# Kernel optimization log

Measured on AMD Instinct MI355X. Metric: run time of the kernel, lower is better.

Reference implementation:

```python
import jax, jax.numpy as jnp
import numpy as np

N_NODES = 100000
N_EDGES = 3200000
IN_DIM, HID_DIM, OUT_DIM = 128, 64, 3


def gcn_conv(x, edge_index, W, b):
    """PyG GCNConv: add self-loops, symmetric deg^{-1/2} normalization,
    linear transform then scatter-sum aggregation, plus bias."""
    n = x.shape[0]
    loop = jnp.arange(n, dtype=edge_index.dtype)
    src = jnp.concatenate([edge_index[0], loop])  # [E+N]
    dst = jnp.concatenate([edge_index[1], loop])
    deg = jax.ops.segment_sum(jnp.ones_like(dst, dtype=x.dtype), dst, num_segments=n)
    dinv = jax.lax.rsqrt(jnp.maximum(deg, 1.0))  # deg >= 1 due to self-loops
    norm = dinv[src] * dinv[dst]                 # [E+N]
    h = x @ W                                    # [N, F_out]
    msgs = h[src] * norm[:, None]                # gather + scale
    out = jax.ops.segment_sum(msgs, dst, num_segments=n)
    return out + b


def setup_inputs() -> dict:
    key = jax.random.key(0)
    k1, k2, k3, k4 = jax.random.split(key, 4)
    x = jax.random.normal(k1, (N_NODES, IN_DIM), dtype=jnp.float32)
    edge_index = jax.random.randint(k2, (2, N_EDGES), 0, N_NODES, dtype=jnp.int64)
    W1 = jax.random.normal(k3, (IN_DIM, HID_DIM), dtype=jnp.float32) * (1.0 / np.sqrt(IN_DIM))
    b1 = jnp.zeros((HID_DIM,), dtype=jnp.float32)
    W2 = jax.random.normal(k4, (HID_DIM, OUT_DIM), dtype=jnp.float32) * (1.0 / np.sqrt(HID_DIM))
    b2 = jnp.zeros((OUT_DIM,), dtype=jnp.float32)
    return {"x": x, "edge_index": edge_index, "W1": W1, "b1": b1, "W2": W2, "b2": b2}


def reference(x, edge_index, W1, b1, W2, b2):
    h = gcn_conv(x, edge_index, W1, b1)
    h = jax.nn.relu(h)
    out = gcn_conv(h, edge_index, W2, b2)
    return out
```

## Files before the change

kernel.cpp:

```cpp
#include <hip/hip_runtime.h>
#include <hip/hip_fp16.h>
#include <cstdint>
#include <cstddef>

#define DIM_IN 128
#define DIM_HID 64
#define MS_TILE 16384
#define OVF_CAP 32768
#define BSH 9
#define BINSZ 512
#define MAXNB 512
#define CAPL 20480

typedef int v2i __attribute__((ext_vector_type(2)));

__global__ __launch_bounds__(1024) void k_msplit3(const int* __restrict__ eidx,
                                                  int* __restrict__ binCursor,
                                                  unsigned int* __restrict__ binned,
                                                  int* __restrict__ ovfCnt,
                                                  v2i* __restrict__ ovf,
                                                  int E, int NB, int cap) {
    __shared__ int hist[256], base[256];
    __shared__ int stF;
    int t = threadIdx.x;
    if (t == 0) {
        int o = 0;
        for (int j = 1; j < 128; j += 2) o |= eidx[j];
        stF = (o == 0) ? 2 : 1;
    }
    __syncthreads();
    int st = stF;
    int ntiles = (E + MS_TILE - 1) / MS_TILE;

    for (int tile = blockIdx.x; tile < ntiles; tile += gridDim.x) {
        int e0 = tile * MS_TILE;
        int e1 = min(e0 + MS_TILE, E);

        if (t < 256) hist[t] = 0;
        __syncthreads();
        for (int e = e0 + t; e < e1; e += 1024) {
            int d = (st == 2) ? ((const v2i*)eidx)[E + e].x : eidx[E + e];
            atomicAdd(&hist[d >> BSH], 1);
        }
        __syncthreads();
        if (t < NB && hist[t] > 0) base[t] = atomicAdd(&binCursor[t], hist[t]);
        __syncthreads();
        if (t < 256) hist[t] = 0;
        __syncthreads();
        for (int e = e0 + t; e < e1; e += 1024) {
            int s, d;
            if (st == 2) {
                s = ((const v2i*)eidx)[e].x;
                d = ((const v2i*)eidx)[E + e].x;
            } else {
                s = eidx[e];
                d = eidx[E + e];
            }
            int b = d >> BSH;
            int r = atomicAdd(&hist[b], 1);
            int local = base[b] + r;
            if (local < cap) {
                binned[(size_t)b * cap + local] =
                    ((unsigned int)s << BSH) | (unsigned int)(d & (BINSZ - 1));
            } else {
                int o = atomicAdd(ovfCnt, 1);
                if (o < OVF_CAP) ovf[o] = (v2i){s, d};
            }
        }
        __syncthreads();
    }
}

__global__ __launch_bounds__(512) void k_binscan(const int* __restrict__ binCursor,
                                                 int* __restrict__ binBase,
                                                 int NB, int cap) {
    __shared__ int sh[512];
    int t = threadIdx.x;
    int v = (t < NB) ? min(binCursor[t], cap) : 0;
    sh[t] = v;
    __syncthreads();
    for (int d = 1; d < 512; d <<= 1) {
        int add = (t >= d) ? sh[t - d] : 0;
        __syncthreads();
        sh[t] += add;
        __syncthreads();
    }
    if (t < NB) binBase[t] = sh[t] - v;
}

__global__ __launch_bounds__(512) void k_fillA(const unsigned int* __restrict__ binned,
                                               const int* __restrict__ binCursor,
                                               const int* __restrict__ binBase,
                                               int* __restrict__ offsets,
                                               int* __restrict__ cursor,
                                               float* __restrict__ dinv,
                                               int* __restrict__ csr,
                                               int cap, int N) {
    __shared__ int hist[BINSZ], scanS[BINSZ], curL[BINSZ];
    __shared__ unsigned int stage[CAPL];
    int b = blockIdx.x;
    int t = threadIdx.x;
    int g0 = b << BSH;
    int g = g0 + t;
    int n = min(binCursor[b], cap);
    const unsigned int* p = binned + (size_t)b * cap;

    hist[t] = 0;
    __syncthreads();
    for (int i = t; i < n; i += 512)
        atomicAdd(&hist[p[i] & (BINSZ - 1)], 1);
    __syncthreads();
    int h = hist[t];
    scanS[t] = h;
    __syncthreads();
    for (int d = 1; d < 512; d <<= 1) {
        int add = (t >= d) ? scanS[t - d] : 0;
        __syncthreads();
        scanS[t] += add;
        __syncthreads();
    }
    int excl = scanS[t] - h;
    int gbase = binBase[b];
    if (g < N) {
        offsets[g] = gbase + excl;
        dinv[g] = rsqrtf((float)(h + 1));
    }
    if (t == 511) offsets[min(g0 + BINSZ, N)] = gbase + scanS[511];

    curL[t] = excl;
    __syncthreads();
    int nl = min(n, CAPL);
    for (int i = t; i < nl; i += 512) {
        unsigned int w = p[i];
        int pos = atomicAdd(&curL[w & (BINSZ - 1)], 1);
        if (pos < CAPL) stage[pos] = w >> BSH;
    }
    __syncthreads();
    if (g < N) cursor[g] = gbase + curL[t];
    for (int i = t; i < nl; i += 512)
        csr[gbase + i] = (int)stage[i];
    __syncthreads();
    for (int i = CAPL + t; i < n; i += 512) {
        unsigned int w = p[i];
        int pos = atomicAdd(&cursor[g0 + (int)(w & (BINSZ - 1))], 1);
        csr[pos] = (int)(w >> BSH);
    }
}

__global__ void k_ovf(const int* __restrict__ ovfCnt, const v2i* __restrict__ ovf,
                      int* __restrict__ cursor, int* __restrict__ csr) {
    int n = min(*ovfCnt, OVF_CAP);
    for (int i = threadIdx.x; i < n; i += 256) {
        v2i e = ovf[i];
        int pos = atomicAdd(&cursor[e.y], 1);
        csr[pos] = e.x;
    }
}

__global__ __launch_bounds__(256) void k_gemm1t(const float* __restrict__ x,
                                                const float* __restrict__ W,
                                                const float* __restrict__ dinv,
                                                __half2* __restrict__ h1, int N) {
    __shared__ __half xsT[DIM_IN * 64];
    __shared__ float Ws[DIM_IN * DIM_HID];
    int t = threadIdx.x;
    int row0 = blockIdx.x * 64;

#pragma unroll
    for (int i = 0; i < 8; i++)
        ((float4*)Ws)[t + 256 * i] = ((const float4*)W)[t + 256 * i];

#pragma unroll
    for (int i = 0; i < 8; i++) {
        int idx = t * 8 + i;
        int r = idx >> 5;
        int kc = idx & 31;
        int row = row0 + r;
        float4 v = (row < N) ? ((const float4*)(x + (size_t)row * DIM_IN))[kc]
                             : make_float4(0.f, 0.f, 0.f, 0.f);
        xsT[(4 * kc + 0) * 64 + r] = __float2half(v.x);
        xsT[(4 * kc + 1) * 64 + r] = __float2half(v.y);
        xsT[(4 * kc + 2) * 64 + r] = __float2half(v.z);
        xsT[(4 * kc + 3) * 64 + r] = __float2half(v.w);
    }
    __syncthreads();

    int c = t & 15;
    int r = t >> 4;
    float acc[4][4] = {};

#pragma unroll 4
    for (int k = 0; k < DIM_IN; k++) {
        __half2 xh01 = *(const __half2*)&xsT[k * 64 + 4 * r];
        __half2 xh23 = *(const __half2*)&xsT[k * 64 + 4 * r + 2];
        float2 x01 = __half22float2(xh01);
        float2 x23 = __half22float2(xh23);
        float4 wb = *(const float4*)&Ws[k * DIM_HID + 4 * c];
        float xi[4] = {x01.x, x01.y, x23.x, x23.y};
#pragma unroll
        for (int i = 0; i < 4; i++) {
            acc[i][0] = fmaf(xi[i], wb.x, acc[i][0]);
            acc[i][1] = fmaf(xi[i], wb.y, acc[i][1]);
            acc[i][2] = fmaf(xi[i], wb.z, acc[i][2]);
            acc[i][3] = fmaf(xi[i], wb.w, acc[i][3]);
        }
    }

#pragma unroll
    for (int i = 0; i < 4; i++) {
        int row = row0 + 4 * r + i;
        if (row < N) {
            float d = dinv[row];
            h1[(size_t)row * 32 + 2 * c] = __floats2half2_rn(acc[i][0] * d, acc[i][1] * d);
            h1[(size_t)row * 32 + 2 * c + 1] = __floats2half2_rn(acc[i][2] * d, acc[i][3] * d);
        }
    }
}

__global__ __launch_bounds__(256) void k_agg1(const __half2* __restrict__ h1,
                                              const int* __restrict__ csr,
                                              const int* __restrict__ offsets,
                                              const float* __restrict__ dinv,
                                              const float* __restrict__ b1,
                                              const float* __restrict__ W2,
                                              float4* __restrict__ h2, int N) {
    int t = threadIdx.x;
    int hl = t & 31;
    int node = blockIdx.x * 8 + (t >> 5);
    if (node >= N) return;

    float di = dinv[node];
    int beg = offsets[node], end = offsets[node + 1];
    __half2 a0 = h1[(size_t)node * 32 + hl];
    __half2 a1 = __floats2half2_rn(0.f, 0.f);

    for (int base = beg; base < end; base += 32) {
        int rem = min(32, end - base);
        int sidx = (hl < rem) ? csr[base + hl] : 0;
        if (rem == 32) {
#pragma unroll
            for (int j0 = 0; j0 < 32; j0 += 8) {
                __half2 v[8];
#pragma unroll
                for (int k = 0; k < 8; k++) {
                    int s = __shfl(sidx, j0 + k, 32);
                    v[k] = h1[(size_t)s * 32 + hl];
                }
#pragma unroll
                for (int k = 0; k < 8; k += 2) {
                    a0 = __hadd2(a0, v[k]);
                    a1 = __hadd2(a1, v[k + 1]);
                }
            }
        } else {
            int j = 0;
            for (; j + 1 < rem; j += 2) {
                int s0 = __shfl(sidx, j, 32);
                int s1 = __shfl(sidx, j + 1, 32);
                a0 = __hadd2(a0, h1[(size_t)s0 * 32 + hl]);
                a1 = __hadd2(a1, h1[(size_t)s1 * 32 + hl]);
            }
            if (j < rem) {
                int s0 = __shfl(sidx, j, 32);
                a0 = __hadd2(a0, h1[(size_t)s0 * 32 + hl]);
            }
        }
    }

    float2 f0 = __half22float2(a0);
    float2 f1 = __half22float2(a1);
    float accx = f0.x + f1.x, accy = f0.y + f1.y;

    float2 bb = ((const float2*)b1)[hl];
    float gx = fmaxf(fmaf(accx, di, bb.x), 0.f);
    float gy = fmaxf(fmaf(accy, di, bb.y), 0.f);

    const float* w0 = W2 + (2 * hl) * 3;
    const float* w1 = W2 + (2 * hl + 1) * 3;
    float v0 = gx * w0[0] + gy * w1[0];
    float v1 = gx * w0[1] + gy * w1[1];
    float v2 = gx * w0[2] + gy * w1[2];
#pragma unroll
    for (int off = 16; off > 0; off >>= 1) {
        v0 += __shfl_xor(v0, off, 64);
        v1 += __shfl_xor(v1, off, 64);
        v2 += __shfl_xor(v2, off, 64);
    }
    if (hl == 0) h2[node] = make_float4(v0 * di, v1 * di, v2 * di, 0.f);
}

__global__ __launch_bounds__(256) void k_agg2(const float4* __restrict__ h2,
                                              const int* __restrict__ csr,
                                              const int* __restrict__ offsets,
                                              const float* __restrict__ dinv,
                                              const float* __restrict__ b2,
                                              float* __restrict__ out, int N) {
    int t = threadIdx.x;
    int l = t & 7;
    int node = blockIdx.x * 32 + (t >> 3);
    if (node >= N) return;

    float di = dinv[node];
    int beg = offsets[node], end = offsets[node + 1];
    float a0 = 0.f, a1 = 0.f, a2 = 0.f;
    for (int e = beg + l; e < end; e += 8) {
        float4 h = h2[csr[e]];
        a0 += h.x;
        a1 += h.y;
        a2 += h.z;
    }
#pragma unroll
    for (int off = 4; off > 0; off >>= 1) {
        a0 += __shfl_xor(a0, off, 8);
        a1 += __shfl_xor(a1, off, 8);
        a2 += __shfl_xor(a2, off, 8);
    }
    if (l == 0) {
        float4 hs = h2[node];
        out[(size_t)node * 3 + 0] = fmaf(a0 + hs.x, di, b2[0]);
        out[(size_t)node * 3 + 1] = fmaf(a1 + hs.y, di, b2[1]);
        out[(size_t)node * 3 + 2] = fmaf(a2 + hs.z, di, b2[2]);
    }
}

extern "C" void kernel_launch(void* const* d_in, const int* in_sizes, int n_in,
                              void* d_out, int out_size, void* d_ws, size_t ws_size,
                              hipStream_t stream) {
    const float* x = (const float*)d_in[0];
    const int* eidx = (const int*)d_in[1];
    const float* W1 = (const float*)d_in[2];
    const float* b1 = (const float*)d_in[3];
    const float* W2 = (const float*)d_in[4];
    const float* b2 = (const float*)d_in[5];
    float* out = (float*)d_out;

    const int N = in_sizes[0] / DIM_IN;
    const int E = in_sizes[1] / 2;
    const int NB = (N + BINSZ - 1) >> BSH;

    char* w = (char*)d_ws;
    size_t off = 0;
    auto carve = [&](size_t bytes) -> char* {
        char* p = w + off;
        off += (bytes + 255) & ~(size_t)255;
        return p;
    };
    int* offsets = (int*)carve((size_t)(N + 1) * 4);
    int* cursor = (int*)carve((size_t)N * 4);
    float* dinv = (float*)carve((size_t)N * 4);
    int* csr = (int*)carve((size_t)E * 4);
    int* binCursor = (int*)carve(MAXNB * 4);
    int* ovfCnt = (int*)carve(16);
    v2i* ovf = (v2i*)carve((size_t)OVF_CAP * 8);
    int* binBase = (int*)carve(MAXNB * 4);
    float4* h2 = (float4*)carve((size_t)N * 16);

    size_t h1_bytes = (size_t)N * DIM_HID * 2;
    int capDes = E / NB + E / NB / 16 + 256;
    size_t binned_des = (size_t)NB * capDes * 4;
    size_t uni_avail = (ws_size > off + 256) ? (ws_size - off - 256) : h1_bytes;
    size_t uni_bytes = binned_des > h1_bytes ? binned_des : h1_bytes;
    if (uni_bytes > uni_avail) uni_bytes = uni_avail > h1_bytes ? uni_avail : h1_bytes;
    char* uni = carve(uni_bytes);
    unsigned int* binned = (unsigned int*)uni;
    __half2* h1 = (__half2*)uni;
    int cap = (int)(uni_bytes / ((size_t)NB * 4));
    if (cap > capDes) cap = capDes;
    if (cap > CAPL) cap = CAPL;

    (void)hipMemsetAsync(binCursor, 0, MAXNB * 4 + 256, stream);

    int ntiles = (E + MS_TILE - 1) / MS_TILE;
    k_msplit3<<<ntiles, 1024, 0, stream>>>(eidx, binCursor, binned, ovfCnt, ovf,
                                           E, NB, cap);
    k_binscan<<<1, 512, 0, stream>>>(binCursor, binBase, NB, cap);
    k_fillA<<<NB, 512, 0, stream>>>(binned, binCursor, binBase, offsets, cursor,
                                    dinv, csr, cap, N);
    k_ovf<<<1, 256, 0, stream>>>(ovfCnt, ovf, cursor, csr);

    k_gemm1t<<<(N + 63) / 64, 256, 0, stream>>>(x, W1, dinv, h1, N);
    k_agg1<<<(N + 7) / 8, 256, 0, stream>>>(h1, csr, offsets, dinv, b1, W2, h2, N);
    k_agg2<<<(N + 31) / 32, 256, 0, stream>>>(h2, csr, offsets, dinv, b2, out, N);
}
```

Measured before the change: 181.1 us.

## Gather h1 rows with 16-byte loads, four neighbors per half-warp group

Restructures the layer-1 aggregation so each 32-lane group splits into four slots of 8 lanes. Each lane loads a uint4 (8 halves), so the group processes four neighbor rows per iteration instead of one 4-byte load per lane per neighbor. Partial sums are combined with xor shuffles before the ReLU/W2 projection, and W2 and b1 are staged in shared memory. This aims to cut the number of memory instructions and raise memory-level parallelism, at the cost of extra shuffles, a block-wide sync and idle lanes on ragged tails.

```diff
diff --git a/kernel.cpp b/kernel.cpp
--- a/kernel.cpp
+++ b/kernel.cpp
@@ -13,6 +13,14 @@
 #define CAPL 20480
 
 typedef int v2i __attribute__((ext_vector_type(2)));
+
+__device__ inline __half2 h2_shfl_xor(__half2 v, int m) {
+    int i = __shfl_xor(*reinterpret_cast<int*>(&v), m, 32);
+    return *reinterpret_cast<__half2*>(&i);
+}
+__device__ inline __half2 u2h(unsigned int u) {
+    return *reinterpret_cast<__half2*>(&u);
+}
 
 __global__ __launch_bounds__(1024) void k_msplit3(const int* __restrict__ eidx,
                                                   int* __restrict__ binCursor,
@@ -224,69 +232,74 @@
                                               const float* __restrict__ b1,
                                               const float* __restrict__ W2,
                                               float4* __restrict__ h2, int N) {
-    int t = threadIdx.x;
+    __shared__ float W2s[DIM_HID * 3];
+    __shared__ float b1s[DIM_HID];
+    int t = threadIdx.x;
+    if (t < DIM_HID * 3) W2s[t] = W2[t];
+    if (t < DIM_HID) b1s[t] = b1[t];
+    __syncthreads();
+
     int hl = t & 31;
+    int slot = hl >> 3;
+    int f8 = hl & 7;
     int node = blockIdx.x * 8 + (t >> 5);
     if (node >= N) return;
 
+    const uint4* h1q = (const uint4*)h1;
     float di = dinv[node];
     int beg = offsets[node], end = offsets[node + 1];
-    __half2 a0 = h1[(size_t)node * 32 + hl];
-    __half2 a1 = __floats2half2_rn(0.f, 0.f);
+
+    __half2 a0, a1, a2, a3;
+    if (slot == 0) {
+        uint4 v = h1q[(size_t)node * 8 + f8];
+        a0 = u2h(v.x); a1 = u2h(v.y); a2 = u2h(v.z); a3 = u2h(v.w);
+    } else {
+        a0 = a1 = a2 = a3 = __floats2half2_rn(0.f, 0.f);
+    }
 
     for (int base = beg; base < end; base += 32) {
-        int rem = min(32, end - base);
-        int sidx = (hl < rem) ? csr[base + hl] : 0;
-        if (rem == 32) {
-#pragma unroll
-            for (int j0 = 0; j0 < 32; j0 += 8) {
-                __half2 v[8];
-#pragma unroll
-                for (int k = 0; k < 8; k++) {
-                    int s = __shfl(sidx, j0 + k, 32);
-                    v[k] = h1[(size_t)s * 32 + hl];
-                }
-#pragma unroll
-                for (int k = 0; k < 8; k += 2) {
-                    a0 = __hadd2(a0, v[k]);
-                    a1 = __hadd2(a1, v[k + 1]);
-                }
+        int cnt = min(32, end - base);
+        int sidx = (hl < cnt) ? csr[base + hl] : 0;
+        int iters = (cnt + 3) >> 2;
+        for (int j = 0; j < iters; j++) {
+            int idx = 4 * j + slot;
+            int s = __shfl(sidx, idx, 32);
+            if (idx < cnt) {
+                uint4 v = h1q[(size_t)s * 8 + f8];
+                a0 = __hadd2(a0, u2h(v.x));
+                a1 = __hadd2(a1, u2h(v.y));
+                a2 = __hadd2(a2, u2h(v.z));
+                a3 = __hadd2(a3, u2h(v.w));
             }
-        } else {
-            int j = 0;
-            for (; j + 1 < rem; j += 2) {
-                int s0 = __shfl(sidx, j, 32);
-                int s1 = __shfl(sidx, j + 1, 32);
-                a0 = __hadd2(a0, h1[(size_t)s0 * 32 + hl]);
-                a1 = __hadd2(a1, h1[(size_t)s1 * 32 + hl]);
-            }
-            if (j < rem) {
-                int s0 = __shfl(sidx, j, 32);
-                a0 = __hadd2(a0, h1[(size_t)s0 * 32 + hl]);
-            }
-        }
-    }
-
-    float2 f0 = __half22float2(a0);
-    float2 f1 = __half22float2(a1);
-    float accx = f0.x + f1.x, accy = f0.y + f1.y;
-
-    float2 bb = ((const float2*)b1)[hl];
-    float gx = fmaxf(fmaf(accx, di, bb.x), 0.f);
-    float gy = fmaxf(fmaf(accy, di, bb.y), 0.f);
-
-    const float* w0 = W2 + (2 * hl) * 3;
-    const float* w1 = W2 + (2 * hl + 1) * 3;
-    float v0 = gx * w0[0] + gy * w1[0];
-    float v1 = gx * w0[1] + gy * w1[1];
-    float v2 = gx * w0[2] + gy * w1[2];
-#pragma unroll
-    for (int off = 16; off > 0; off >>= 1) {
-        v0 += __shfl_xor(v0, off, 64);
-        v1 += __shfl_xor(v1, off, 64);
-        v2 += __shfl_xor(v2, off, 64);
-    }
-    if (hl == 0) h2[node] = make_float4(v0 * di, v1 * di, v2 * di, 0.f);
+        }
+    }
+
+    a0 = __hadd2(a0, h2_shfl_xor(a0, 8));  a0 = __hadd2(a0, h2_shfl_xor(a0, 16));
+    a1 = __hadd2(a1, h2_shfl_xor(a1, 8));  a1 = __hadd2(a1, h2_shfl_xor(a1, 16));
+    a2 = __hadd2(a2, h2_shfl_xor(a2, 8));  a2 = __hadd2(a2, h2_shfl_xor(a2, 16));
+    a3 = __hadd2(a3, h2_shfl_xor(a3, 8));  a3 = __hadd2(a3, h2_shfl_xor(a3, 16));
+
+    if (slot == 0) {
+        float2 f0 = __half22float2(a0), f1 = __half22float2(a1);
+        float2 f2 = __half22float2(a2), f3 = __half22float2(a3);
+        float acc[8] = {f0.x, f0.y, f1.x, f1.y, f2.x, f2.y, f3.x, f3.y};
+        float v0 = 0.f, v1 = 0.f, v2 = 0.f;
+#pragma unroll
+        for (int k = 0; k < 8; k++) {
+            int f = 8 * f8 + k;
+            float gg = fmaxf(fmaf(acc[k], di, b1s[f]), 0.f);
+            v0 = fmaf(gg, W2s[f * 3 + 0], v0);
+            v1 = fmaf(gg, W2s[f * 3 + 1], v1);
+            v2 = fmaf(gg, W2s[f * 3 + 2], v2);
+        }
+#pragma unroll
+        for (int off = 4; off > 0; off >>= 1) {
+            v0 += __shfl_xor(v0, off, 8);
+            v1 += __shfl_xor(v1, off, 8);
+            v2 += __shfl_xor(v2, off, 8);
+        }
+        if (f8 == 0) h2[node] = make_float4(v0 * di, v1 * di, v2 * di, 0.f);
+    }
 }
 
 __global__ __launch_bounds__(256) void k_agg2(const float4* __restrict__ h2,
```

New measurement: 174.8 us. 1.04x faster.
